# Optimization experiments

Hardware: AMD Instinct MI355X
Metric: run time of the kernel (lower is better)

The kernel has to match this reference:

```python
import jax, jax.numpy as jnp
import numpy as np

N_NODES = 100000
N_EDGES = 50000
NNZ = 3200000
D = 32
ALPHA = 0.5


def setup_inputs() -> dict:
    key = jax.random.key(0)
    ks = jax.random.split(key, 10)
    X = jax.random.normal(ks[0], (N_NODES, D), dtype=jnp.float32)
    X0 = jax.random.normal(ks[1], (N_NODES, D), dtype=jnp.float32)
    atts = jax.random.uniform(ks[2], (NNZ, 1), dtype=jnp.float32)
    vertex = jax.random.randint(ks[3], (NNZ,), 0, N_NODES)
    edges = jnp.sort(jax.random.randint(ks[4], (NNZ,), 0, N_EDGES))
    s = 1.0 / np.sqrt(D)
    # Linear params stored as [in, out]
    W1_w = jax.random.uniform(ks[5], (D, D), jnp.float32, -s, s)
    W1_b = jnp.zeros((D,), jnp.float32)
    s2 = 1.0 / np.sqrt(2 * D)
    W2_w = jax.random.uniform(ks[6], (2 * D, D), jnp.float32, -s2, s2)
    W2_b = jnp.zeros((D,), jnp.float32)
    W_w = jax.random.uniform(ks[7], (D, D), jnp.float32, -s, s)
    W_b = jnp.zeros((D,), jnp.float32)
    return {"X": X, "X0": X0, "atts": atts,
            "W1_w": W1_w, "W1_b": W1_b, "W2_w": W2_w, "W2_b": W2_b,
            "W_w": W_w, "W_b": W_b, "vertex": vertex, "edges": edges}


def reference(X, X0, atts, W1_w, W1_b, W2_w, W2_b, W_w, W_b, vertex, edges):
    # EquivSetConv.forward (eval mode, 1-layer MLPs, aggr='add')
    N = X.shape[0]
    # W1(X) then gather to incidences: [nnz, D]
    X1 = X @ W1_w + W1_b
    Xve = X1[vertex] * atts  # atts [nnz,1] broadcasts over D (torch expand(-1,32))
    # scatter-add over hyperedges: [n_edges, D]
    Xe = jax.ops.segment_sum(Xve, edges, num_segments=N_EDGES)
    # gather back per incidence and mix with source node features
    Xev = jnp.concatenate([X[vertex], Xe[edges]], axis=-1)  # [nnz, 2D]
    Xev = Xev @ W2_w + W2_b  # [nnz, D]
    # scatter-add back to nodes
    Xv = jax.ops.segment_sum(Xev, vertex, num_segments=N)
    Xr = (1.0 - ALPHA) * Xv + ALPHA * X0
    return Xr @ W_w + W_b
```

## Files before the change

kernel.cpp:

```cpp
#include <hip/hip_runtime.h>
#include <hip/hip_fp16.h>

#define N_NODES 100000
#define N_EDGES 50000
#define NNZ     3200000
#define D       32
#define NB      782
#define BSH     7
#define BMSK    127u
#define PCAP    4480
#define SLOTS   72
#define P1_CHUNK 4096
#define P1_T     1024
#define P1_BLKS  ((NNZ + P1_CHUNK - 1) / P1_CHUNK)
#define P2_T     512

#define PRE_XH_BLKS   3125
#define PRE_SEG_BLKS  196
#define PRE_BCUR_BLK  (PRE_XH_BLKS + PRE_SEG_BLKS)
#define PRE_K0_BLK0   (PRE_BCUR_BLK + 1)
#define PRE_BLKS      (PRE_K0_BLK0 + 4)

typedef _Float16 half8 __attribute__((ext_vector_type(8)));
typedef float    f32x4 __attribute__((ext_vector_type(4)));
typedef float    f32x2 __attribute__((ext_vector_type(2)));

__device__ __forceinline__ unsigned int pkadd(unsigned int a, unsigned int b) {
    __half2 r = __hadd2(*(__half2*)&a, *(__half2*)&b);
    return *(unsigned int*)&r;
}

__global__ void k_pre(const float* __restrict__ X, unsigned int* __restrict__ Xh8,
                      const int* __restrict__ edges, int* __restrict__ seg,
                      unsigned int* __restrict__ bcur,
                      const float* __restrict__ W1, const float* __restrict__ b1,
                      const float* __restrict__ W2, const float* __restrict__ b2,
                      const float* __restrict__ Ww,
                      _Float16* __restrict__ M1t, _Float16* __restrict__ A2t,
                      _Float16* __restrict__ Wt,
                      float* __restrict__ c1, float* __restrict__ c2) {
    int blk = blockIdx.x, t = threadIdx.x;
    if (blk < PRE_XH_BLKS) {
        int i = blk * 256 + t;
        float4 v = ((const float4*)X)[i];
        unsigned int d = 0;
        d = __builtin_amdgcn_cvt_pk_fp8_f32(v.x, v.y, d, false);
        d = __builtin_amdgcn_cvt_pk_fp8_f32(v.z, v.w, d, true);
        Xh8[i] = d;
    } else if (blk < PRE_BCUR_BLK) {
        int e = (blk - PRE_XH_BLKS) * 256 + t;
        if (e <= N_EDGES) {
            int lo = 0, hi = NNZ;
            while (lo < hi) { int mid = (lo + hi) >> 1; if (edges[mid] < e) lo = mid + 1; else hi = mid; }
            seg[e] = lo;
        }
    } else if (blk == PRE_BCUR_BLK) {
        for (int i = t; i < NB; i += 256) bcur[i] = (unsigned)(i * PCAP);
    } else {
        int k  = (blk - PRE_K0_BLK0) * 8 + (t >> 5);
        int dd = t & 31;
        float m = 0.f, a = 0.f;
#pragma unroll
        for (int j = 0; j < D; ++j) {
            m = fmaf(W1[k * D + j], W2[(D + j) * D + dd], m);
            a = fmaf(W2[k * D + j], Ww[j * D + dd], a);
        }
        M1t[dd * D + k] = (_Float16)m;
        A2t[dd * D + k] = (_Float16)(0.5f * a);
        Wt[dd * D + k]  = (_Float16)(0.5f * Ww[k * D + dd]);
        if (k == 0) {
            float cc1 = 0.f, cc2 = 0.f;
#pragma unroll
            for (int j = 0; j < D; ++j) {
                cc1 = fmaf(b1[j], W2[(D + j) * D + dd], cc1);
                cc2 = fmaf(b2[j], Ww[j * D + dd], cc2);
            }
            c1[dd] = cc1;
            c2[dd] = cc2;
        }
    }
}

__global__ __launch_bounds__(P1_T) void p1(const int* __restrict__ vertex,
                                           const int* __restrict__ edges,
                                           unsigned int* __restrict__ bcur,
                                           unsigned int* __restrict__ plist) {
    __shared__ unsigned int cnt[NB], excl[NB], cursor[NB], gbase[NB];
    __shared__ unsigned int wsum[16];
    __shared__ unsigned int obuf[P1_CHUNK];
    __shared__ unsigned short obb[P1_CHUNK];
    int t = threadIdx.x;
    int wv = t >> 6, lane = t & 63;
    int c0 = blockIdx.x * P1_CHUNK;
    int cend = min(c0 + P1_CHUNK, NNZ);

    for (int i = t; i < NB; i += P1_T) cnt[i] = 0;
    __syncthreads();
    for (int i = c0 + t; i < cend; i += P1_T)
        atomicAdd(&cnt[((unsigned)vertex[i]) >> BSH], 1u);
    __syncthreads();

    unsigned int myc = (t < NB) ? cnt[t] : 0;
    unsigned int v = myc;
#pragma unroll
    for (int off = 1; off < 64; off <<= 1) {
        unsigned int u = __shfl_up(v, off, 64);
        if (lane >= off) v += u;
    }
    if (lane == 63) wsum[wv] = v;
    __syncthreads();
    if (t < 16) {
        unsigned int x = wsum[t];
#pragma unroll
        for (int off = 1; off < 16; off <<= 1) {
            unsigned int u = __shfl_up(x, off, 64);
            if (t >= off) x += u;
        }
        wsum[t] = x;
    }
    __syncthreads();
    unsigned int wbase = (wv == 0) ? 0u : wsum[wv - 1];
    unsigned int ex = v + wbase - myc;
    if (t < NB) {
        excl[t] = ex; cursor[t] = ex;
        gbase[t] = myc ? atomicAdd(&bcur[t], myc) : 0u;
    }
    __syncthreads();

    for (int i = c0 + t; i < cend; i += P1_T) {
        unsigned int vv = (unsigned)vertex[i];
        unsigned int e = (unsigned)edges[i];
        unsigned int b = vv >> BSH;
        unsigned int p = atomicAdd(&cursor[b], 1u);
        obuf[p] = (e << BSH) | (vv & BMSK);
        obb[p]  = (unsigned short)b;
    }
    __syncthreads();

    int csize = cend - c0;
    for (int j = t; j < csize; j += P1_T) {
        unsigned int b = obb[j];
        plist[gbase[b] + (j - excl[b])] = obuf[j];
    }
}

__global__ __launch_bounds__(1024) void k2f(const unsigned int* __restrict__ Xh8,
                                            const float* __restrict__ atts,
                                            const int* __restrict__ vertex,
                                            const int* __restrict__ seg,
                                            const _Float16* __restrict__ M1t,
                                            const float* __restrict__ c1,
                                            unsigned int* __restrict__ FeU) {
    __shared__ unsigned int yebuf[16][16];
    __shared__ float sas[16];
    int t = threadIdx.x;
    int wave = t >> 6;
    int lane = t & 63;
    int e = blockIdx.x * 16 + wave;

    int start = seg[e];
    int len   = seg[e + 1] - start;
    int k16   = lane >> 2;
    int h4    = lane & 3;

    float a0 = 0.f, a1 = 0.f, a2 = 0.f, a3 = 0.f;
    float a4 = 0.f, a5 = 0.f, a6 = 0.f, a7 = 0.f;
    float sa = 0.f;

    for (int base = 0; base < len; base += 64) {
        int off = base + lane;
        int vv = 0; float aa = 0.f;
        if (off < len) { vv = vertex[start + off]; aa = atts[start + off]; }
#pragma unroll
        for (int g = 0; g < 4; ++g) {
            int   vk = __shfl(vv, g * 16 + k16, 64);
            float ak = __shfl(aa, g * 16 + k16, 64);
            uint2 w = *(const uint2*)(Xh8 + vk * 8 + h4 * 2);
            f32x2 p0 = __builtin_amdgcn_cvt_pk_f32_fp8(w.x, false);
            f32x2 p1 = __builtin_amdgcn_cvt_pk_f32_fp8(w.x, true);
            f32x2 p2 = __builtin_amdgcn_cvt_pk_f32_fp8(w.y, false);
            f32x2 p3 = __builtin_amdgcn_cvt_pk_f32_fp8(w.y, true);
            a0 = fmaf(ak, p0.x, a0); a1 = fmaf(ak, p0.y, a1);
            a2 = fmaf(ak, p1.x, a2); a3 = fmaf(ak, p1.y, a3);
            a4 = fmaf(ak, p2.x, a4); a5 = fmaf(ak, p2.y, a5);
            a6 = fmaf(ak, p3.x, a6); a7 = fmaf(ak, p3.y, a7);
            sa += ak;
        }
    }

    __half2 q0 = __floats2half2_rn(a0, a1), q1 = __floats2half2_rn(a2, a3);
    __half2 q2 = __floats2half2_rn(a4, a5), q3 = __floats2half2_rn(a6, a7);
    unsigned int u0 = *(unsigned int*)&q0, u1 = *(unsigned int*)&q1;
    unsigned int u2 = *(unsigned int*)&q2, u3 = *(unsigned int*)&q3;
#pragma unroll
    for (int m = 4; m < 64; m <<= 1) {
        u0 = pkadd(u0, __shfl_xor(u0, m, 64));
        u1 = pkadd(u1, __shfl_xor(u1, m, 64));
        u2 = pkadd(u2, __shfl_xor(u2, m, 64));
        u3 = pkadd(u3, __shfl_xor(u3, m, 64));
        sa += __shfl_xor(sa, m, 64);
    }
    if (k16 == 0) {
        uint4 w; w.x = u0; w.y = u1; w.z = u2; w.w = u3;
        *(uint4*)(&yebuf[wave][h4 * 4]) = w;
    }
    if (lane == 0) sas[wave] = sa;
    __syncthreads();

    if (wave != 0) return;
    int m0 = blockIdx.x * 16;
    int n  = lane & 15, g = lane >> 4;
    const _Float16* yb = (const _Float16*)yebuf;
    half8 af = *(const half8*)(yb + n * D + g * 8);
    f32x4 z = {0.f, 0.f, 0.f, 0.f};

#pragma unroll
    for (int cb = 0; cb < 2; ++cb) {
        int ng = cb * 16 + n;
        half8 bf = *(const half8*)(M1t + ng * D + g * 8);
        f32x4 acc = __builtin_amdgcn_mfma_f32_16x16x32_f16(af, bf, z, 0, 0, 0);
        float c1n = c1[ng];
#pragma unroll
        for (int r = 0; r < 4; ++r) {
            int lr = g * 4 + r;
            float val = acc[r] + sas[lr] * c1n;
            float other = __shfl(val, lane ^ 1, 64);
            if ((n & 1) == 0) {
                __half2 hv = __floats2half2_rn(val, other);
                FeU[(m0 + lr) * 16 + (ng >> 1)] = *(unsigned int*)&hv;
            }
        }
    }
}

__global__ __launch_bounds__(P2_T) void p2(const unsigned int* __restrict__ plist,
                                           const unsigned int* __restrict__ FeU,
                                           const unsigned int* __restrict__ bcur,
                                           unsigned int* __restrict__ SfU,
                                           unsigned int* __restrict__ nodedeg) {
    __shared__ unsigned int sbuf[128 * SLOTS];
    __shared__ unsigned int cursor[128];
    int t = threadIdx.x;
    if (t < 128) cursor[t] = 0;
    __syncthreads();

    int b = blockIdx.x;
    int base = b << BSH;
    int start = b * PCAP;
    int n = (int)bcur[b] - start;

    for (int i = t; i < n; i += P2_T) {
        unsigned int ent = plist[start + i];
        unsigned int lv = ent & BMSK;
        unsigned int p = atomicAdd(&cursor[lv], 1u);
        sbuf[lv * SLOTS + p] = ent >> BSH;
    }
    __syncthreads();

    int hw = t >> 5, lane = t & 31;
    int k8 = lane >> 2;
    int h4 = lane & 3;
    for (int r = 0; r < 8; ++r) {
        int ln = r * 16 + hw;
        int node = base + ln;
        if (node >= N_NODES) continue;
        int deg = (int)cursor[ln];
        const unsigned int* nbuf = sbuf + ln * SLOTS;

        unsigned int a0 = 0u, a1 = 0u, a2 = 0u, a3 = 0u;
        unsigned int a4 = 0u, a5 = 0u, a6 = 0u, a7 = 0u;
        for (int j0 = 0; j0 < deg; j0 += 16) {
            int iA = j0 + k8, iB = j0 + 8 + k8;
            bool vA = (iA < deg), vB = (iB < deg);
            unsigned int eA = vA ? nbuf[iA] : 0u;
            unsigned int eB = vB ? nbuf[iB] : 0u;
            uint4 wA = *(const uint4*)(FeU + eA * 16 + h4 * 4);
            uint4 wB = *(const uint4*)(FeU + eB * 16 + h4 * 4);
            if (!vA) { wA.x = 0u; wA.y = 0u; wA.z = 0u; wA.w = 0u; }
            if (!vB) { wB.x = 0u; wB.y = 0u; wB.z = 0u; wB.w = 0u; }
            a0 = pkadd(a0, wA.x); a1 = pkadd(a1, wA.y);
            a2 = pkadd(a2, wA.z); a3 = pkadd(a3, wA.w);
            a4 = pkadd(a4, wB.x); a5 = pkadd(a5, wB.y);
            a6 = pkadd(a6, wB.z); a7 = pkadd(a7, wB.w);
        }
        a0 = pkadd(a0, a4); a1 = pkadd(a1, a5);
        a2 = pkadd(a2, a6); a3 = pkadd(a3, a7);
#pragma unroll
        for (int m = 4; m < 32; m <<= 1) {
            a0 = pkadd(a0, __shfl_xor(a0, m, 32));
            a1 = pkadd(a1, __shfl_xor(a1, m, 32));
            a2 = pkadd(a2, __shfl_xor(a2, m, 32));
            a3 = pkadd(a3, __shfl_xor(a3, m, 32));
        }
        if (k8 == 0) {
            uint4 w; w.x = a0; w.y = a1; w.z = a2; w.w = a3;
            *(uint4*)(SfU + node * 16 + h4 * 4) = w;
        }
        if (lane == 0) nodedeg[node] = (unsigned)deg;
    }
}

__global__ __launch_bounds__(256) void k3(const float* __restrict__ X,
                                          const float* __restrict__ X0,
                                          const unsigned int* __restrict__ SfU,
                                          const unsigned int* __restrict__ nodedeg,
                                          const _Float16* __restrict__ A2t,
                                          const _Float16* __restrict__ Wt,
                                          const float* __restrict__ c2,
                                          const float* __restrict__ bw,
                                          float* __restrict__ out) {
    int wg = blockIdx.x * 4 + (threadIdx.x >> 6);
    if (wg >= N_NODES / 16) return;
    int m0 = wg * 16;
    int l  = threadIdx.x & 63;
    int n  = l & 15, g = l >> 4;
    int row = m0 + n;

    const float4* xr = (const float4*)(X + (size_t)row * D);
    float4 xa = xr[g * 2], xb = xr[g * 2 + 1];
    half8 xf = { (_Float16)xa.x, (_Float16)xa.y, (_Float16)xa.z, (_Float16)xa.w,
                 (_Float16)xb.x, (_Float16)xb.y, (_Float16)xb.z, (_Float16)xb.w };

    const __half2* sfp = (const __half2*)(SfU + (size_t)row * 16 + g * 4);
    const float4* x0r = (const float4*)(X0 + (size_t)row * D);
    float4 ya = x0r[g * 2], yb = x0r[g * 2 + 1];
    __half2 s0 = sfp[0], s1 = sfp[1], s2h = sfp[2], s3 = sfp[3];
    half8 tf = { (_Float16)(__low2float(s0) + ya.x),  (_Float16)(__high2float(s0) + ya.y),
                 (_Float16)(__low2float(s1) + ya.z),  (_Float16)(__high2float(s1) + ya.w),
                 (_Float16)(__low2float(s2h) + yb.x), (_Float16)(__high2float(s2h) + yb.y),
                 (_Float16)(__low2float(s3) + yb.z),  (_Float16)(__high2float(s3) + yb.w) };

    f32x4 z = {0.f, 0.f, 0.f, 0.f};
#pragma unroll
    for (int cb = 0; cb < 2; ++cb) {
        int ng = cb * 16 + n;
        half8 a2f = *(const half8*)(A2t + ng * D + g * 8);
        half8 wf  = *(const half8*)(Wt  + ng * D + g * 8);
        f32x4 acc1 = __builtin_amdgcn_mfma_f32_16x16x32_f16(xf, a2f, z, 0, 0, 0);
        f32x4 acc2 = __builtin_amdgcn_mfma_f32_16x16x32_f16(tf, wf,  z, 0, 0, 0);
        float hc2 = 0.5f * c2[ng];
        float bwn = bw[ng];
#pragma unroll
        for (int r = 0; r < 4; ++r) {
            int mr = m0 + g * 4 + r;
            float degf = (float)nodedeg[mr];
            out[(size_t)mr * D + ng] = fmaf(degf, acc1[r] + hc2, acc2[r] + bwn);
        }
    }
}

extern "C" void kernel_launch(void* const* d_in, const int* in_sizes, int n_in,
                              void* d_out, int out_size, void* d_ws, size_t ws_size,
                              hipStream_t stream) {
    const float* X      = (const float*)d_in[0];
    const float* X0     = (const float*)d_in[1];
    const float* atts   = (const float*)d_in[2];
    const float* W1w    = (const float*)d_in[3];
    const float* W1b    = (const float*)d_in[4];
    const float* W2w    = (const float*)d_in[5];
    const float* W2b    = (const float*)d_in[6];
    const float* Ww     = (const float*)d_in[7];
    const float* Wb     = (const float*)d_in[8];
    const int*   vertex = (const int*)d_in[9];
    const int*   edges  = (const int*)d_in[10];
    float*       out    = (float*)d_out;

    char* ws = (char*)d_ws;
    unsigned int* FeU     = (unsigned int*)(ws);
    unsigned int* plist   = (unsigned int*)(ws + 3200000);
    unsigned int* Xh8     = (unsigned int*)(ws + 17208320);
    unsigned int* SfU     = (unsigned int*)(ws + 20408320);
    int*          seg     = (int*)         (ws + 26808320);
    unsigned int* bcur    = (unsigned int*)(ws + 27008512);
    unsigned int* nodedeg = (unsigned int*)(ws + 27011712);
    _Float16*     M1t     = (_Float16*)    (ws + 27411712);
    _Float16*     A2t     = (_Float16*)    (ws + 27413760);
    _Float16*     Wt      = (_Float16*)    (ws + 27415808);
    float*        c1      = (float*)       (ws + 27417856);
    float*        c2      = (float*)       (ws + 27417984);

    k_pre <<<PRE_BLKS, 256, 0, stream>>>(X, Xh8, edges, seg, bcur,
                                         W1w, W1b, W2w, W2b, Ww, M1t, A2t, Wt, c1, c2);
    p1    <<<P1_BLKS, P1_T, 0, stream>>>(vertex, edges, bcur, plist);
    k2f   <<<N_EDGES / 16, 1024, 0, stream>>>(Xh8, atts, vertex, seg, M1t, c1, FeU);
    p2    <<<NB, P2_T, 0, stream>>>(plist, FeU, bcur, SfU, nodedeg);
    k3    <<<(N_NODES / 16 + 3) / 4, 256, 0, stream>>>(X, X0, SfU, nodedeg,
                                                       A2t, Wt, c2, Wb, out);
}
```

Measured before the change: 111.4 us.

## Fuse node gather kernel with final MFMA output projection via shared memory

Merges the per-node gather/sum kernel (p2) with the final output kernel (k3), so each block's 128 node sums stay in LDS instead of going to a global SfU buffer. Node degrees come straight from the LDS cursor array, so the nodedeg buffer is gone too. This removes a kernel launch and a global write and read of the intermediate. It adds LDS use per block, which may lower occupancy, and the MFMA epilogue now runs after the gather phase inside the same block.

```diff
diff --git a/kernel.cpp b/kernel.cpp
--- a/kernel.cpp
+++ b/kernel.cpp
@@ -14,6 +14,7 @@
 #define P1_T     1024
 #define P1_BLKS  ((NNZ + P1_CHUNK - 1) / P1_CHUNK)
 #define P2_T     512
+#define SFP      20
 
 #define PRE_XH_BLKS   3125
 #define PRE_SEG_BLKS  196
@@ -233,12 +234,18 @@
     }
 }
 
-__global__ __launch_bounds__(P2_T) void p2(const unsigned int* __restrict__ plist,
-                                           const unsigned int* __restrict__ FeU,
-                                           const unsigned int* __restrict__ bcur,
-                                           unsigned int* __restrict__ SfU,
-                                           unsigned int* __restrict__ nodedeg) {
+__global__ __launch_bounds__(P2_T) void p2full(const unsigned int* __restrict__ plist,
+                                               const unsigned int* __restrict__ FeU,
+                                               const unsigned int* __restrict__ bcur,
+                                               const float* __restrict__ X,
+                                               const float* __restrict__ X0,
+                                               const _Float16* __restrict__ A2t,
+                                               const _Float16* __restrict__ Wt,
+                                               const float* __restrict__ c2,
+                                               const float* __restrict__ bw,
+                                               float* __restrict__ out) {
     __shared__ unsigned int sbuf[128 * SLOTS];
+    __shared__ unsigned int sfb[128 * SFP];
     __shared__ unsigned int cursor[128];
     int t = threadIdx.x;
     if (t < 128) cursor[t] = 0;
@@ -263,7 +270,7 @@
     for (int r = 0; r < 8; ++r) {
         int ln = r * 16 + hw;
         int node = base + ln;
-        if (node >= N_NODES) continue;
+        if (node >= N_NODES) { if (k8 == 0) { uint4 zz = {0,0,0,0}; *(uint4*)(&sfb[ln * SFP + h4 * 4]) = zz; } continue; }
         int deg = (int)cursor[ln];
         const unsigned int* nbuf = sbuf + ln * SLOTS;
 
@@ -294,37 +301,28 @@
         }
         if (k8 == 0) {
             uint4 w; w.x = a0; w.y = a1; w.z = a2; w.w = a3;
-            *(uint4*)(SfU + node * 16 + h4 * 4) = w;
-        }
-        if (lane == 0) nodedeg[node] = (unsigned)deg;
-    }
-}
-
-__global__ __launch_bounds__(256) void k3(const float* __restrict__ X,
-                                          const float* __restrict__ X0,
-                                          const unsigned int* __restrict__ SfU,
-                                          const unsigned int* __restrict__ nodedeg,
-                                          const _Float16* __restrict__ A2t,
-                                          const _Float16* __restrict__ Wt,
-                                          const float* __restrict__ c2,
-                                          const float* __restrict__ bw,
-                                          float* __restrict__ out) {
-    int wg = blockIdx.x * 4 + (threadIdx.x >> 6);
-    if (wg >= N_NODES / 16) return;
-    int m0 = wg * 16;
-    int l  = threadIdx.x & 63;
-    int n  = l & 15, g = l >> 4;
-    int row = m0 + n;
-
-    const float4* xr = (const float4*)(X + (size_t)row * D);
+            *(uint4*)(&sfb[ln * SFP + h4 * 4]) = w;
+        }
+    }
+    __syncthreads();
+
+    int wv = t >> 6;
+    int l  = t & 63;
+    int nn = l & 15, g = l >> 4;
+    int ln0 = wv * 16 + nn;
+    int row = base + ln0;
+    int rowc = min(row, N_NODES - 1);
+
+    const float4* xr = (const float4*)(X + (size_t)rowc * D);
     float4 xa = xr[g * 2], xb = xr[g * 2 + 1];
     half8 xf = { (_Float16)xa.x, (_Float16)xa.y, (_Float16)xa.z, (_Float16)xa.w,
                  (_Float16)xb.x, (_Float16)xb.y, (_Float16)xb.z, (_Float16)xb.w };
 
-    const __half2* sfp = (const __half2*)(SfU + (size_t)row * 16 + g * 4);
-    const float4* x0r = (const float4*)(X0 + (size_t)row * D);
+    uint4 sw = *(const uint4*)(&sfb[ln0 * SFP + g * 4]);
+    __half2 s0 = *(__half2*)&sw.x, s1 = *(__half2*)&sw.y;
+    __half2 s2h = *(__half2*)&sw.z, s3 = *(__half2*)&sw.w;
+    const float4* x0r = (const float4*)(X0 + (size_t)rowc * D);
     float4 ya = x0r[g * 2], yb = x0r[g * 2 + 1];
-    __half2 s0 = sfp[0], s1 = sfp[1], s2h = sfp[2], s3 = sfp[3];
     half8 tf = { (_Float16)(__low2float(s0) + ya.x),  (_Float16)(__high2float(s0) + ya.y),
                  (_Float16)(__low2float(s1) + ya.z),  (_Float16)(__high2float(s1) + ya.w),
                  (_Float16)(__low2float(s2h) + yb.x), (_Float16)(__high2float(s2h) + yb.y),
@@ -333,7 +331,7 @@
     f32x4 z = {0.f, 0.f, 0.f, 0.f};
 #pragma unroll
     for (int cb = 0; cb < 2; ++cb) {
-        int ng = cb * 16 + n;
+        int ng = cb * 16 + nn;
         half8 a2f = *(const half8*)(A2t + ng * D + g * 8);
         half8 wf  = *(const half8*)(Wt  + ng * D + g * 8);
         f32x4 acc1 = __builtin_amdgcn_mfma_f32_16x16x32_f16(xf, a2f, z, 0, 0, 0);
@@ -342,9 +340,12 @@
         float bwn = bw[ng];
 #pragma unroll
         for (int r = 0; r < 4; ++r) {
-            int mr = m0 + g * 4 + r;
-            float degf = (float)nodedeg[mr];
-            out[(size_t)mr * D + ng] = fmaf(degf, acc1[r] + hc2, acc2[r] + bwn);
+            int lnr = wv * 16 + g * 4 + r;
+            int mr = base + lnr;
+            if (mr < N_NODES) {
+                float degf = (float)cursor[lnr];
+                out[(size_t)mr * D + ng] = fmaf(degf, acc1[r] + hc2, acc2[r] + bwn);
+            }
         }
     }
 }
@@ -366,24 +367,20 @@
     float*       out    = (float*)d_out;
 
     char* ws = (char*)d_ws;
-    unsigned int* FeU     = (unsigned int*)(ws);
-    unsigned int* plist   = (unsigned int*)(ws + 3200000);
-    unsigned int* Xh8     = (unsigned int*)(ws + 17208320);
-    unsigned int* SfU     = (unsigned int*)(ws + 20408320);
-    int*          seg     = (int*)         (ws + 26808320);
-    unsigned int* bcur    = (unsigned int*)(ws + 27008512);
-    unsigned int* nodedeg = (unsigned int*)(ws + 27011712);
-    _Float16*     M1t     = (_Float16*)    (ws + 27411712);
-    _Float16*     A2t     = (_Float16*)    (ws + 27413760);
-    _Float16*     Wt      = (_Float16*)    (ws + 27415808);
-    float*        c1      = (float*)       (ws + 27417856);
-    float*        c2      = (float*)       (ws + 27417984);
+    unsigned int* FeU   = (unsigned int*)(ws);
+    unsigned int* plist = (unsigned int*)(ws + 3200000);
+    unsigned int* Xh8   = (unsigned int*)(ws + 17208320);
+    int*          seg   = (int*)         (ws + 20408320);
+    unsigned int* bcur  = (unsigned int*)(ws + 20608512);
+    _Float16*     M1t   = (_Float16*)    (ws + 20611712);
+    _Float16*     A2t   = (_Float16*)    (ws + 20613760);
+    _Float16*     Wt    = (_Float16*)    (ws + 20615808);
+    float*        c1    = (float*)       (ws + 20617856);
+    float*        c2    = (float*)       (ws + 20617984);
 
     k_pre <<<PRE_BLKS, 256, 0, stream>>>(X, Xh8, edges, seg, bcur,
                                          W1w, W1b, W2w, W2b, Ww, M1t, A2t, Wt, c1, c2);
     p1    <<<P1_BLKS, P1_T, 0, stream>>>(vertex, edges, bcur, plist);
     k2f   <<<N_EDGES / 16, 1024, 0, stream>>>(Xh8, atts, vertex, seg, M1t, c1, FeU);
-    p2    <<<NB, P2_T, 0, stream>>>(plist, FeU, bcur, SfU, nodedeg);
-    k3    <<<(N_NODES / 16 + 3) / 4, 256, 0, stream>>>(X, X0, SfU, nodedeg,
-                                                       A2t, Wt, c2, Wb, out);
-}
+    p2full<<<NB, P2_T, 0, stream>>>(plist, FeU, bcur, X, X0, A2t, Wt, c2, Wb, out);
+}
```

New measurement: 117.3 us. 5.3% more time.
